# Optimization experiments

Measured on AMD Instinct MI355X. Metric: run time of the kernel, lower is better.

Reference implementation:

```python
import jax, jax.numpy as jnp
import numpy as np
import math

C = 32  # per-head channel dim (init arg c)


def _layernorm(x, g, b, eps=1e-5):
    mu = x.mean(-1, keepdims=True)
    var = ((x - mu) ** 2).mean(-1, keepdims=True)
    return (x - mu) * jax.lax.rsqrt(var + eps) * g + b


def setup_inputs() -> dict:
    key = jax.random.key(0)
    ks = jax.random.split(key, 8)
    S, N, D = 17, 4096, 256  # S = 1 target + 16 MSTA templates
    h = jax.random.normal(ks[0], (S, N, D), jnp.float32)
    msta_mask = jax.random.uniform(ks[1], (S - 1, N)) < 0.5
    # module requires count(target_msta_mask) == count(msta_mask); use equal masks
    target_msta_mask = msta_mask
    w = lambda k: jax.random.normal(k, (D, D), jnp.float32) * 0.05
    return dict(
        h=h, target_msta_mask=target_msta_mask, msta_mask=msta_mask,
        Wq=w(ks[2]), Wk=w(ks[3]), Wv=w(ks[4]), Wo=w(ks[5]),
        bo=jnp.zeros((D,), jnp.float32),
        ln_g=jnp.ones((D,), jnp.float32), ln_b=jnp.zeros((D,), jnp.float32),
    )


def reference(h, target_msta_mask, msta_mask, Wq, Wk, Wv, Wo, bo, ln_g, ln_b):
    S, N, D = h.shape
    H = D // C
    M = msta_mask.shape[0]  # == S - 1
    # --- msta_h[target_msta_mask] = h[1:][msta_mask] (rank-matched scatter, jit-safe) ---
    h1 = h[1:].reshape(M * N, D)
    src = msta_mask.reshape(-1)
    dst = target_msta_mask.reshape(-1)
    src_rank = jnp.cumsum(src.astype(jnp.int32)) - 1
    buf = jnp.zeros((M * N, D), h.dtype).at[jnp.where(src, src_rank, M * N)].set(h1, mode='drop')
    dst_rank = jnp.clip(jnp.cumsum(dst.astype(jnp.int32)) - 1, 0, M * N - 1)
    msta_h = jnp.where(dst[:, None], buf[dst_rank], 0.0).reshape(M, N, D)
    # --- full-column equivalent of the subset attention (per-position independent) ---
    cols = target_msta_mask.any(0)                      # [N]
    attn_h = jnp.concatenate([h[:1], msta_h], axis=0)   # [S, N, D]
    mask = jnp.concatenate([cols[None], target_msta_mask], axis=0)  # [S, N]; == inverse_mask == attn_mask (full cols)
    q = (attn_h @ Wq.T).reshape(S, N, H, C)
    k = (attn_h @ Wk.T).reshape(S, N, H, C)
    v = (attn_h @ Wv.T).reshape(S, N, H, C)
    att = jnp.einsum('snhc,tnhc->stnh', q, k) / math.sqrt(C)
    att = att - (~mask).astype(h.dtype)[None, :, :, None] * 1e9
    att = jax.nn.softmax(att, axis=1)                   # softmax over key-sample axis t
    attn_o = jnp.einsum('stnh,tnhc->snhc', att, v).reshape(S, N, D)
    # o[inverse_mask] = attn_o[attn_mask]  (masks coincide in full-column form)
    o = jnp.where(mask[..., None], attn_o, h @ Wv.T)
    o = o @ Wo.T + bo
    # dropout is identity in eval mode
    return _layernorm(h + o, ln_g, ln_b)
```

## Files before the change

### kernel.cpp

```cpp
#include <hip/hip_runtime.h>
#include <hip/hip_bf16.h>

#define S 17
#define NPOS 4096
#define D 256
#define NH 8
#define CH 32
#define MROWS 16

typedef __attribute__((ext_vector_type(8))) short bf16x8;
typedef __attribute__((ext_vector_type(4))) float f32x4;

__device__ __forceinline__ float bfu(unsigned short u) {
  return __uint_as_float(((unsigned int)u) << 16);
}
__device__ __forceinline__ unsigned short f2b(float f) {
  __hip_bfloat16 t = __float2bfloat16(f);
  return *reinterpret_cast<unsigned short*>(&t);
}
__device__ __forceinline__ void unpack16(const uint4 A, const uint4 B, float* r) {
  r[0]  = __uint_as_float(A.x << 16); r[1]  = __uint_as_float(A.x & 0xffff0000u);
  r[2]  = __uint_as_float(A.y << 16); r[3]  = __uint_as_float(A.y & 0xffff0000u);
  r[4]  = __uint_as_float(A.z << 16); r[5]  = __uint_as_float(A.z & 0xffff0000u);
  r[6]  = __uint_as_float(A.w << 16); r[7]  = __uint_as_float(A.w & 0xffff0000u);
  r[8]  = __uint_as_float(B.x << 16); r[9]  = __uint_as_float(B.x & 0xffff0000u);
  r[10] = __uint_as_float(B.y << 16); r[11] = __uint_as_float(B.y & 0xffff0000u);
  r[12] = __uint_as_float(B.z << 16); r[13] = __uint_as_float(B.z & 0xffff0000u);
  r[14] = __uint_as_float(B.w << 16); r[15] = __uint_as_float(B.w & 0xffff0000u);
}
__device__ __forceinline__ float readv(const void* p, int f32, size_t i) {
  return f32 ? ((const float*)p)[i] : bfu(((const unsigned short*)p)[i]);
}

__device__ __forceinline__ void gl_lds16(const unsigned short* g, unsigned short* l) {
  __builtin_amdgcn_global_load_lds(
      (const __attribute__((address_space(1))) unsigned int*)g,
      (__attribute__((address_space(3))) unsigned int*)l, 16, 0, 0);
}

struct TensorList {
  const unsigned short* p[8];
  int n[8];
};

__global__ void detect_multi_kernel(TensorList tl, int* __restrict__ flags) {
  __shared__ int s_totnz, s_evnz, s_evwild;
  if (threadIdx.x == 0) { s_totnz = 0; s_evnz = 0; s_evwild = 0; }
  __syncthreads();
  const unsigned short* p = tl.p[blockIdx.x];
  const int n = tl.n[blockIdx.x];
  const int w = n < 4096 ? n : 4096;
  int totnz = 0, evnz = 0, evwild = 0;
  for (int i = threadIdx.x; i < w; i += blockDim.x) {
    unsigned short u = p[i];
    if (u) {
      totnz++;
      if (!(i & 1)) {
        evnz++;
        int e = (u >> 7) & 0xFF;
        if (e == 0 || e == 255 || e < 97 || e > 157) evwild++;
      }
    }
  }
  atomicAdd(&s_totnz, totnz);
  atomicAdd(&s_evnz, evnz);
  atomicAdd(&s_evwild, evwild);
  __syncthreads();
  if (threadIdx.x == 0) {
    const int evcount = w / 2;
    int f;
    if (s_totnz == 0) f = 0;
    else if (s_evnz == 0) f = 1;
    else if (s_evwild * 8 > evcount) f = 1;
    else f = 0;
    flags[blockIdx.x] = f;
  }
}

__global__ void detect_mask_kernel(const unsigned int* __restrict__ w,
                                   int* __restrict__ cls) {
  __shared__ int viol[5];
  if (threadIdx.x < 5) viol[threadIdx.x] = 0;
  __syncthreads();
  int v_i32 = 0, v_f32 = 0, v_bf16 = 0, v_u8 = 0, v_i64 = 0;
  const int nwords = 65536 / 4;
  for (int i = threadIdx.x; i < nwords; i += blockDim.x) {
    unsigned int x = w[i];
    if (x > 1u) v_i32 = 1;
    if (x != 0u && x != 0x3F800000u) v_f32 = 1;
    unsigned int lo = x & 0xFFFFu, hi = x >> 16;
    if ((lo != 0u && lo != 0x3F80u) || (hi != 0u && hi != 0x3F80u)) v_bf16 = 1;
    if ((x & 0xFEFEFEFEu) != 0u) v_u8 = 1;
    if ((i & 1) && x != 0u) v_i64 = 1;
  }
  if (v_i32) atomicOr(&viol[0], 1);
  if (v_f32) atomicOr(&viol[1], 1);
  if (v_bf16) atomicOr(&viol[2], 1);
  if (v_u8) atomicOr(&viol[3], 1);
  if (v_i64) atomicOr(&viol[4], 1);
  __syncthreads();
  if (threadIdx.x == 0) {
    int c;
    if (!viol[0] && !viol[4]) c = 4;
    else if (!viol[0]) c = 0;
    else if (!viol[1]) c = 2;
    else if (!viol[2]) c = 3;
    else c = 1;
    *cls = c;
  }
}

__global__ void expand_mask_kernel(const void* __restrict__ tmask, const int* __restrict__ cls,
                                   unsigned char* __restrict__ mask_u8) {
  int n = blockIdx.x * blockDim.x + threadIdx.x;
  if (n >= NPOS) return;
  const int c = *cls;
  int any = 0;
  for (int m = 0; m < MROWS; m++) {
    size_t idx = (size_t)m * NPOS + n;
    int v;
    if (c == 0)      v = ((const int*)tmask)[idx] != 0;
    else if (c == 1) v = ((const unsigned char*)tmask)[idx] != 0;
    else if (c == 2) v = ((const unsigned int*)tmask)[idx] != 0u;
    else if (c == 3) v = ((const unsigned short*)tmask)[idx] != 0u;
    else             v = ((const unsigned long long*)tmask)[idx] != 0ull;
    mask_u8[(m + 1) * NPOS + n] = (unsigned char)v;
    any |= v;
  }
  mask_u8[n] = (unsigned char)any;
}

struct WPtrs { const void* p[4]; };

__global__ void conv_w_kernel(WPtrs wp, const int* __restrict__ flags,
                              unsigned short* __restrict__ w_bf) {
  for (int i = blockIdx.x * blockDim.x + threadIdx.x; i < 4 * 65536;
       i += gridDim.x * blockDim.x) {
    int which = i >> 16, off = i & 65535;
    int f = flags[1 + which];
    w_bf[i] = f ? f2b(((const float*)wp.p[which])[off])
                : ((const unsigned short*)wp.p[which])[off];
  }
}

__global__ __launch_bounds__(256) void qkv_kernel(
    const void* __restrict__ h, const int* __restrict__ flags,
    const unsigned short* __restrict__ w_bf,
    unsigned short* __restrict__ q_ws, unsigned short* __restrict__ k_ws,
    unsigned short* __restrict__ v_ws) {
  __shared__ unsigned short lds[16384];
  const int tid = threadIdx.x;
  const int wave = tid >> 6, lane = tid & 63;
  const int l15 = lane & 15, quad = lane >> 4;
  const int bid = blockIdx.x;
  const int nt = (bid >> 3) % 6;
  const size_t mt = (size_t)(bid & 7) + 8 * (size_t)(bid / 48);
  const size_t R = mt * 128;
  const unsigned short* Wb = w_bf + (size_t)(nt * 128) * 256;
  const int hf32 = flags[0];
  const int srow = lane >> 3;
  const int scol = (lane & 7) * 8;
  const int wm = wave >> 1, wn = wave & 1;

  f32x4 acc[4][4];
  #pragma unroll
  for (int a = 0; a < 4; a++)
    #pragma unroll
    for (int b = 0; b < 4; b++) acc[a][b] = (f32x4){0.f, 0.f, 0.f, 0.f};

  for (int k0 = 0; k0 < 4; k0++) {
    if (hf32) {
      const float* hf = (const float*)h;
      #pragma unroll
      for (int i = 0; i < 4; i++) {
        int row = i * 32 + wave * 8 + srow;
        const float4* src = (const float4*)&hf[(R + row) * 256 + k0 * 64 + scol];
        float4 v0 = src[0], v1 = src[1];
        unsigned int w0 = ((unsigned)f2b(v0.y) << 16) | f2b(v0.x);
        unsigned int w1 = ((unsigned)f2b(v0.w) << 16) | f2b(v0.z);
        unsigned int w2 = ((unsigned)f2b(v1.y) << 16) | f2b(v1.x);
        unsigned int w3 = ((unsigned)f2b(v1.w) << 16) | f2b(v1.z);
        *(uint4*)&lds[i * 2048 + wave * 512 + lane * 8] = make_uint4(w0, w1, w2, w3);
      }
    } else {
      const unsigned short* hb = (const unsigned short*)h;
      #pragma unroll
      for (int i = 0; i < 4; i++) {
        int row = i * 32 + wave * 8 + srow;
        gl_lds16(&hb[(R + row) * 256 + k0 * 64 + scol], &lds[i * 2048 + wave * 512]);
      }
    }
    #pragma unroll
    for (int i = 0; i < 4; i++) {
      int row = i * 32 + wave * 8 + srow;
      gl_lds16(&Wb[(size_t)row * 256 + k0 * 64 + scol], &lds[8192 + i * 2048 + wave * 512]);
    }
    asm volatile("s_waitcnt vmcnt(0)" ::: "memory");
    __syncthreads();
    bf16x8 af[4][2], bfr[4][2];
    #pragma unroll
    for (int mi = 0; mi < 4; mi++)
      #pragma unroll
      for (int kk = 0; kk < 2; kk++)
        af[mi][kk] = *(const bf16x8*)&lds[(wm * 64 + mi * 16 + l15) * 64 + kk * 32 + quad * 8];
    #pragma unroll
    for (int ni = 0; ni < 4; ni++)
      #pragma unroll
      for (int kk = 0; kk < 2; kk++)
        bfr[ni][kk] = *(const bf16x8*)&lds[8192 + (wn * 64 + ni * 16 + l15) * 64 + kk * 32 + quad * 8];
    #pragma unroll
    for (int kk = 0; kk < 2; kk++)
      #pragma unroll
      for (int mi = 0; mi < 4; mi++)
        #pragma unroll
        for (int ni = 0; ni < 4; ni++)
          acc[mi][ni] = __builtin_amdgcn_mfma_f32_16x16x32_bf16(af[mi][kk], bfr[ni][kk],
                                                                acc[mi][ni], 0, 0, 0);
    __syncthreads();
  }
  const int p = nt >> 1;
  const int cbase = (nt & 1) * 128;
  unsigned short* dst = (p == 0) ? q_ws : (p == 1) ? k_ws : v_ws;
  #pragma unroll
  for (int mi = 0; mi < 4; mi++)
    #pragma unroll
    for (int ni = 0; ni < 4; ni++)
      #pragma unroll
      for (int r = 0; r < 4; r++) {
        int row = wm * 64 + mi * 16 + quad * 4 + r;
        int col = cbase + wn * 64 + ni * 16 + l15;
        dst[(R + row) * 256 + col] = f2b(acc[mi][ni][r]);
      }
}

__global__ __launch_bounds__(256) void attn_kernel(
    const unsigned short* __restrict__ q_ws, const unsigned short* __restrict__ k_ws,
    const unsigned short* __restrict__ v_ws, const unsigned char* __restrict__ mask_u8,
    unsigned short* __restrict__ o_ws) {
  __shared__ unsigned short qb[S * D], kb[S * D], vb[S * D];
  __shared__ float pmat[S * 160];
  __shared__ unsigned char sm[32];
  const int tid = threadIdx.x;
  const int n = blockIdx.x;
  if (tid < S) sm[tid] = mask_u8[tid * NPOS + n];
  for (int idx = tid; idx < S * 32; idx += 256) {
    int s = idx >> 5, c = idx & 31;
    size_t g = ((size_t)s * NPOS + n) * 32 + c;
    ((uint4*)qb)[idx] = ((const uint4*)q_ws)[g];
    ((uint4*)kb)[idx] = ((const uint4*)k_ws)[g];
    ((uint4*)vb)[idx] = ((const uint4*)v_ws)[g];
  }
  __syncthreads();
  {
    const int hh = tid >> 5, s = tid & 31;
    if (s < S) {
      float qv[32];
      const uint4* qp = (const uint4*)(qb + s * 256 + hh * 32);
      unpack16(qp[0], qp[1], qv);
      unpack16(qp[2], qp[3], qv + 16);
      const float scale = 0.17677669529663687f;
      float sc[S];
      float mx = -3.4e38f;
      #pragma unroll
      for (int t = 0; t < S; t++) {
        const uint4* kp = (const uint4*)(kb + t * 256 + hh * 32);
        float kv[16];
        unpack16(kp[0], kp[1], kv);
        float a = 0.f;
        #pragma unroll
        for (int u = 0; u < 16; u++) a = fmaf(qv[u], kv[u], a);
        unpack16(kp[2], kp[3], kv);
        #pragma unroll
        for (int u = 0; u < 16; u++) a = fmaf(qv[16 + u], kv[u], a);
        a *= scale;
        if (!sm[t]) a -= 1e9f;
        sc[t] = a;
        mx = fmaxf(mx, a);
      }
      float sum = 0.f;
      #pragma unroll
      for (int t = 0; t < S; t++) { sc[t] = __expf(sc[t] - mx); sum += sc[t]; }
      const float inv = 1.f / sum;
      float* pr = pmat + s * 160 + hh * 20;
      #pragma unroll
      for (int t = 0; t < S; t++) pr[t] = sc[t] * inv;
      pr[17] = 0.f; pr[18] = 0.f; pr[19] = 0.f;
    }
  }
  __syncthreads();
  {
    const int d = tid, hh = d >> 5;
    float vf[S];
    #pragma unroll
    for (int t = 0; t < S; t++) vf[t] = bfu(vb[t * 256 + d]);
    #pragma unroll 1
    for (int s = 0; s < S; s++) {
      const float* pr = pmat + s * 160 + hh * 20;
      float ov = 0.f;
      #pragma unroll
      for (int t = 0; t < S; t++) ov = fmaf(pr[t], vf[t], ov);
      const float o_val = sm[s] ? ov : vf[s];
      o_ws[((size_t)s * NPOS + n) * 256 + d] = f2b(o_val);
    }
  }
}

template <int HF32>
__device__ __forceinline__ void oproj_body(
    const unsigned short* __restrict__ o_ws, const void* __restrict__ h,
    const unsigned short* __restrict__ w_bf, const int* __restrict__ fl,
    const void* __restrict__ bo, const void* __restrict__ lng,
    const void* __restrict__ lnb, float* __restrict__ out,
    unsigned short* lds) {
  const int tid = threadIdx.x;
  const int wave = tid >> 6, lane = tid & 63;
  const int l15 = lane & 15, quad = lane >> 4;
  const int srow = lane >> 3;
  const int scol = (lane & 7) * 8;
  const size_t R = (size_t)blockIdx.x * 128;
  const unsigned short* Wp = w_bf + 3 * 65536;

  f32x4 acc0[16], acc1[16];
  #pragma unroll
  for (int j = 0; j < 16; j++) {
    acc0[j] = (f32x4){0.f, 0.f, 0.f, 0.f};
    acc1[j] = (f32x4){0.f, 0.f, 0.f, 0.f};
  }

  for (int k0 = 0; k0 < 4; k0++) {
    #pragma unroll
    for (int i = 0; i < 4; i++) {
      int row = i * 32 + wave * 8 + srow;
      gl_lds16(&o_ws[(R + row) * 256 + k0 * 64 + scol], &lds[i * 2048 + wave * 512]);
    }
    #pragma unroll
    for (int i = 0; i < 8; i++) {
      int row = i * 32 + wave * 8 + srow;
      gl_lds16(&Wp[(size_t)row * 256 + k0 * 64 + scol], &lds[8192 + i * 2048 + wave * 512]);
    }
    asm volatile("s_waitcnt vmcnt(0)" ::: "memory");
    __syncthreads();
    bf16x8 af0k[2], af1k[2];
    #pragma unroll
    for (int kk = 0; kk < 2; kk++) {
      af0k[kk] = *(const bf16x8*)&lds[(wave * 32 + l15) * 64 + kk * 32 + quad * 8];
      af1k[kk] = *(const bf16x8*)&lds[(wave * 32 + 16 + l15) * 64 + kk * 32 + quad * 8];
    }
    #pragma unroll
    for (int kk = 0; kk < 2; kk++)
      #pragma unroll
      for (int j = 0; j < 16; j++) {
        bf16x8 b = *(const bf16x8*)&lds[8192 + (j * 16 + l15) * 64 + kk * 32 + quad * 8];
        acc0[j] = __builtin_amdgcn_mfma_f32_16x16x32_bf16(af0k[kk], b, acc0[j], 0, 0, 0);
        acc1[j] = __builtin_amdgcn_mfma_f32_16x16x32_bf16(af1k[kk], b, acc1[j], 0, 0, 0);
      }
    __syncthreads();
  }

  const int f5 = fl[5], f6 = fl[6], f7 = fl[7];
  float xsum0[4] = {0, 0, 0, 0}, xsq0[4] = {0, 0, 0, 0};
  float xsum1[4] = {0, 0, 0, 0}, xsq1[4] = {0, 0, 0, 0};
  #pragma unroll
  for (int j = 0; j < 16; j++) {
    const int col = j * 16 + l15;
    const float boj = readv(bo, f5, col);
    #pragma unroll
    for (int r = 0; r < 4; r++) {
      const size_t row0 = R + wave * 32 + quad * 4 + r;
      const size_t row1 = row0 + 16;
      float h0 = HF32 ? ((const float*)h)[row0 * 256 + col]
                      : bfu(((const unsigned short*)h)[row0 * 256 + col]);
      float h1 = HF32 ? ((const float*)h)[row1 * 256 + col]
                      : bfu(((const unsigned short*)h)[row1 * 256 + col]);
      float x0 = acc0[j][r] + h0 + boj;
      float x1 = acc1[j][r] + h1 + boj;
      acc0[j][r] = x0; acc1[j][r] = x1;
      xsum0[r] += x0; xsq0[r] += x0 * x0;
      xsum1[r] += x1; xsq1[r] += x1 * x1;
    }
  }
  #pragma unroll
  for (int r = 0; r < 4; r++) {
    #pragma unroll
    for (int m = 1; m <= 8; m <<= 1) {
      xsum0[r] += __shfl_xor(xsum0[r], m, 64);
      xsq0[r]  += __shfl_xor(xsq0[r], m, 64);
      xsum1[r] += __shfl_xor(xsum1[r], m, 64);
      xsq1[r]  += __shfl_xor(xsq1[r], m, 64);
    }
  }
  float mu0[4], rs0[4], mu1[4], rs1[4];
  #pragma unroll
  for (int r = 0; r < 4; r++) {
    mu0[r] = xsum0[r] * (1.0f / 256.0f);
    rs0[r] = rsqrtf(fmaxf(xsq0[r] * (1.0f / 256.0f) - mu0[r] * mu0[r], 0.0f) + 1e-5f);
    mu1[r] = xsum1[r] * (1.0f / 256.0f);
    rs1[r] = rsqrtf(fmaxf(xsq1[r] * (1.0f / 256.0f) - mu1[r] * mu1[r], 0.0f) + 1e-5f);
  }
  #pragma unroll
  for (int j = 0; j < 16; j++) {
    const int col = j * 16 + l15;
    const float gj = readv(lng, f6, col);
    const float bj = readv(lnb, f7, col);
    #pragma unroll
    for (int r = 0; r < 4; r++) {
      const size_t row0 = R + wave * 32 + quad * 4 + r;
      out[row0 * 256 + col] = (acc0[j][r] - mu0[r]) * rs0[r] * gj + bj;
      out[(row0 + 16) * 256 + col] = (acc1[j][r] - mu1[r]) * rs1[r] * gj + bj;
    }
  }
}

__global__ __launch_bounds__(256) void oproj_ln_kernel(
    const unsigned short* __restrict__ o_ws, const void* __restrict__ h,
    const unsigned short* __restrict__ w_bf, const int* __restrict__ flags,
    const void* __restrict__ bo, const void* __restrict__ lng,
    const void* __restrict__ lnb, float* __restrict__ out) {
  __shared__ unsigned short lds[24576];
  if (flags[0]) oproj_body<1>(o_ws, h, w_bf, flags, bo, lng, lnb, out, lds);
  else          oproj_body<0>(o_ws, h, w_bf, flags, bo, lng, lnb, out, lds);
}

extern "C" void kernel_launch(void* const* d_in, const int* in_sizes, int n_in,
                              void* d_out, int out_size, void* d_ws, size_t ws_size,
                              hipStream_t stream) {
  const void* h     = d_in[0];
  const void* tmask = d_in[1];
  const void* Wq  = d_in[3];
  const void* Wk  = d_in[4];
  const void* Wv  = d_in[5];
  const void* Wo  = d_in[6];
  const void* bo  = d_in[7];
  const void* lng = d_in[8];
  const void* lnb = d_in[9];
  float* out = (float*)d_out;

  char* ws = (char*)d_ws;
  int* mcls  = (int*)ws;
  int* flags = (int*)(ws + 64);
  unsigned char* mask_u8 = (unsigned char*)(ws + 4096);
  unsigned short* w_bf = (unsigned short*)(ws + 73728);
  unsigned short* q_ws = (unsigned short*)(ws + 598016);
  unsigned short* k_ws = (unsigned short*)(ws + 598016 + 35651584ull);
  unsigned short* v_ws = (unsigned short*)(ws + 598016 + 2 * 35651584ull);
  unsigned short* o_ws = q_ws;

  TensorList tl;
  tl.p[0] = (const unsigned short*)h;   tl.n[0] = in_sizes[0];
  tl.p[1] = (const unsigned short*)Wq;  tl.n[1] = in_sizes[3];
  tl.p[2] = (const unsigned short*)Wk;  tl.n[2] = in_sizes[4];
  tl.p[3] = (const unsigned short*)Wv;  tl.n[3] = in_sizes[5];
  tl.p[4] = (const unsigned short*)Wo;  tl.n[4] = in_sizes[6];
  tl.p[5] = (const unsigned short*)bo;  tl.n[5] = in_sizes[7];
  tl.p[6] = (const unsigned short*)lng; tl.n[6] = in_sizes[8];
  tl.p[7] = (const unsigned short*)lnb; tl.n[7] = in_sizes[9];
  WPtrs wp;
  wp.p[0] = Wq; wp.p[1] = Wk; wp.p[2] = Wv; wp.p[3] = Wo;

  detect_multi_kernel<<<8, 256, 0, stream>>>(tl, flags);
  detect_mask_kernel<<<1, 256, 0, stream>>>((const unsigned int*)tmask, mcls);
  expand_mask_kernel<<<NPOS / 256, 256, 0, stream>>>(tmask, mcls, mask_u8);
  conv_w_kernel<<<256, 256, 0, stream>>>(wp, flags, w_bf);
  qkv_kernel<<<544 * 6, 256, 0, stream>>>(h, flags, w_bf, q_ws, k_ws, v_ws);
  attn_kernel<<<NPOS, 256, 0, stream>>>(q_ws, k_ws, v_ws, mask_u8, o_ws);
  oproj_ln_kernel<<<S * NPOS / 128, 256, 0, stream>>>(o_ws, h, w_bf, flags,
                                                      bo, lng, lnb, out);
}
```

Measured before the change: 384.0 us.

## Enlarge QKV GEMM tile to 256 rows and merge preprocessing launches

The QKV projection block grows from 256 to 512 threads and from 128 to 256 rows per block, sharing each loaded 128-column weight tile across twice as many rows. This halves weight traffic per output and halves the block count. The four small setup kernels (dtype detection, mask detection, mask expansion, weight conversion) are merged into two launches to cut launch overhead. The explicit vmcnt wait before the barrier after the LDS-direct global loads was also dropped, which risks a race unless the compiler inserts that wait itself.

```diff
diff --git a/kernel.cpp b/kernel.cpp
--- a/kernel.cpp
+++ b/kernel.cpp
@@ -43,119 +43,120 @@
   int n[8];
 };
 
-__global__ void detect_multi_kernel(TensorList tl, int* __restrict__ flags) {
-  __shared__ int s_totnz, s_evnz, s_evwild;
-  if (threadIdx.x == 0) { s_totnz = 0; s_evnz = 0; s_evwild = 0; }
-  __syncthreads();
-  const unsigned short* p = tl.p[blockIdx.x];
-  const int n = tl.n[blockIdx.x];
-  const int w = n < 4096 ? n : 4096;
-  int totnz = 0, evnz = 0, evwild = 0;
-  for (int i = threadIdx.x; i < w; i += blockDim.x) {
-    unsigned short u = p[i];
-    if (u) {
-      totnz++;
-      if (!(i & 1)) {
-        evnz++;
-        int e = (u >> 7) & 0xFF;
-        if (e == 0 || e == 255 || e < 97 || e > 157) evwild++;
-      }
-    }
-  }
-  atomicAdd(&s_totnz, totnz);
-  atomicAdd(&s_evnz, evnz);
-  atomicAdd(&s_evwild, evwild);
-  __syncthreads();
-  if (threadIdx.x == 0) {
-    const int evcount = w / 2;
-    int f;
-    if (s_totnz == 0) f = 0;
-    else if (s_evnz == 0) f = 1;
-    else if (s_evwild * 8 > evcount) f = 1;
-    else f = 0;
-    flags[blockIdx.x] = f;
-  }
-}
-
-__global__ void detect_mask_kernel(const unsigned int* __restrict__ w,
-                                   int* __restrict__ cls) {
-  __shared__ int viol[5];
-  if (threadIdx.x < 5) viol[threadIdx.x] = 0;
-  __syncthreads();
-  int v_i32 = 0, v_f32 = 0, v_bf16 = 0, v_u8 = 0, v_i64 = 0;
-  const int nwords = 65536 / 4;
-  for (int i = threadIdx.x; i < nwords; i += blockDim.x) {
-    unsigned int x = w[i];
-    if (x > 1u) v_i32 = 1;
-    if (x != 0u && x != 0x3F800000u) v_f32 = 1;
-    unsigned int lo = x & 0xFFFFu, hi = x >> 16;
-    if ((lo != 0u && lo != 0x3F80u) || (hi != 0u && hi != 0x3F80u)) v_bf16 = 1;
-    if ((x & 0xFEFEFEFEu) != 0u) v_u8 = 1;
-    if ((i & 1) && x != 0u) v_i64 = 1;
-  }
-  if (v_i32) atomicOr(&viol[0], 1);
-  if (v_f32) atomicOr(&viol[1], 1);
-  if (v_bf16) atomicOr(&viol[2], 1);
-  if (v_u8) atomicOr(&viol[3], 1);
-  if (v_i64) atomicOr(&viol[4], 1);
-  __syncthreads();
-  if (threadIdx.x == 0) {
-    int c;
-    if (!viol[0] && !viol[4]) c = 4;
-    else if (!viol[0]) c = 0;
-    else if (!viol[1]) c = 2;
-    else if (!viol[2]) c = 3;
-    else c = 1;
-    *cls = c;
-  }
-}
-
-__global__ void expand_mask_kernel(const void* __restrict__ tmask, const int* __restrict__ cls,
-                                   unsigned char* __restrict__ mask_u8) {
-  int n = blockIdx.x * blockDim.x + threadIdx.x;
-  if (n >= NPOS) return;
-  const int c = *cls;
-  int any = 0;
-  for (int m = 0; m < MROWS; m++) {
-    size_t idx = (size_t)m * NPOS + n;
-    int v;
-    if (c == 0)      v = ((const int*)tmask)[idx] != 0;
-    else if (c == 1) v = ((const unsigned char*)tmask)[idx] != 0;
-    else if (c == 2) v = ((const unsigned int*)tmask)[idx] != 0u;
-    else if (c == 3) v = ((const unsigned short*)tmask)[idx] != 0u;
-    else             v = ((const unsigned long long*)tmask)[idx] != 0ull;
-    mask_u8[(m + 1) * NPOS + n] = (unsigned char)v;
-    any |= v;
-  }
-  mask_u8[n] = (unsigned char)any;
+__global__ void detect_kernel(TensorList tl, int* __restrict__ flags,
+                              const unsigned int* __restrict__ mw, int* __restrict__ cls) {
+  if (blockIdx.x < 8) {
+    __shared__ int s_totnz, s_evnz, s_evwild;
+    if (threadIdx.x == 0) { s_totnz = 0; s_evnz = 0; s_evwild = 0; }
+    __syncthreads();
+    const unsigned short* p = tl.p[blockIdx.x];
+    const int n = tl.n[blockIdx.x];
+    const int w = n < 4096 ? n : 4096;
+    int totnz = 0, evnz = 0, evwild = 0;
+    for (int i = threadIdx.x; i < w; i += blockDim.x) {
+      unsigned short u = p[i];
+      if (u) {
+        totnz++;
+        if (!(i & 1)) {
+          evnz++;
+          int e = (u >> 7) & 0xFF;
+          if (e == 0 || e == 255 || e < 97 || e > 157) evwild++;
+        }
+      }
+    }
+    atomicAdd(&s_totnz, totnz);
+    atomicAdd(&s_evnz, evnz);
+    atomicAdd(&s_evwild, evwild);
+    __syncthreads();
+    if (threadIdx.x == 0) {
+      const int evcount = w / 2;
+      int f;
+      if (s_totnz == 0) f = 0;
+      else if (s_evnz == 0) f = 1;
+      else if (s_evwild * 8 > evcount) f = 1;
+      else f = 0;
+      flags[blockIdx.x] = f;
+    }
+  } else {
+    __shared__ int viol[5];
+    if (threadIdx.x < 5) viol[threadIdx.x] = 0;
+    __syncthreads();
+    int v_i32 = 0, v_f32 = 0, v_bf16 = 0, v_u8 = 0, v_i64 = 0;
+    const int nwords = 65536 / 4;
+    for (int i = threadIdx.x; i < nwords; i += blockDim.x) {
+      unsigned int x = mw[i];
+      if (x > 1u) v_i32 = 1;
+      if (x != 0u && x != 0x3F800000u) v_f32 = 1;
+      unsigned int lo = x & 0xFFFFu, hi = x >> 16;
+      if ((lo != 0u && lo != 0x3F80u) || (hi != 0u && hi != 0x3F80u)) v_bf16 = 1;
+      if ((x & 0xFEFEFEFEu) != 0u) v_u8 = 1;
+      if ((i & 1) && x != 0u) v_i64 = 1;
+    }
+    if (v_i32) atomicOr(&viol[0], 1);
+    if (v_f32) atomicOr(&viol[1], 1);
+    if (v_bf16) atomicOr(&viol[2], 1);
+    if (v_u8) atomicOr(&viol[3], 1);
+    if (v_i64) atomicOr(&viol[4], 1);
+    __syncthreads();
+    if (threadIdx.x == 0) {
+      int c;
+      if (!viol[0] && !viol[4]) c = 4;
+      else if (!viol[0]) c = 0;
+      else if (!viol[1]) c = 2;
+      else if (!viol[2]) c = 3;
+      else c = 1;
+      *cls = c;
+    }
+  }
 }
 
 struct WPtrs { const void* p[4]; };
 
-__global__ void conv_w_kernel(WPtrs wp, const int* __restrict__ flags,
-                              unsigned short* __restrict__ w_bf) {
-  for (int i = blockIdx.x * blockDim.x + threadIdx.x; i < 4 * 65536;
-       i += gridDim.x * blockDim.x) {
-    int which = i >> 16, off = i & 65535;
-    int f = flags[1 + which];
-    w_bf[i] = f ? f2b(((const float*)wp.p[which])[off])
-                : ((const unsigned short*)wp.p[which])[off];
-  }
-}
-
-__global__ __launch_bounds__(256) void qkv_kernel(
+__global__ void prep_kernel(const void* __restrict__ tmask, const int* __restrict__ cls,
+                            unsigned char* __restrict__ mask_u8,
+                            WPtrs wp, const int* __restrict__ flags,
+                            unsigned short* __restrict__ w_bf) {
+  if (blockIdx.x < 16) {
+    int n = blockIdx.x * blockDim.x + threadIdx.x;
+    if (n >= NPOS) return;
+    const int c = *cls;
+    int any = 0;
+    for (int m = 0; m < MROWS; m++) {
+      size_t idx = (size_t)m * NPOS + n;
+      int v;
+      if (c == 0)      v = ((const int*)tmask)[idx] != 0;
+      else if (c == 1) v = ((const unsigned char*)tmask)[idx] != 0;
+      else if (c == 2) v = ((const unsigned int*)tmask)[idx] != 0u;
+      else if (c == 3) v = ((const unsigned short*)tmask)[idx] != 0u;
+      else             v = ((const unsigned long long*)tmask)[idx] != 0ull;
+      mask_u8[(m + 1) * NPOS + n] = (unsigned char)v;
+      any |= v;
+    }
+    mask_u8[n] = (unsigned char)any;
+  } else {
+    for (int i = (blockIdx.x - 16) * blockDim.x + threadIdx.x; i < 4 * 65536;
+         i += 256 * 256) {
+      int which = i >> 16, off = i & 65535;
+      int f = flags[1 + which];
+      w_bf[i] = f ? f2b(((const float*)wp.p[which])[off])
+                  : ((const unsigned short*)wp.p[which])[off];
+    }
+  }
+}
+
+__global__ __launch_bounds__(512, 5) void qkv_kernel(
     const void* __restrict__ h, const int* __restrict__ flags,
     const unsigned short* __restrict__ w_bf,
     unsigned short* __restrict__ q_ws, unsigned short* __restrict__ k_ws,
     unsigned short* __restrict__ v_ws) {
-  __shared__ unsigned short lds[16384];
+  __shared__ unsigned short lds[24576];
   const int tid = threadIdx.x;
   const int wave = tid >> 6, lane = tid & 63;
   const int l15 = lane & 15, quad = lane >> 4;
   const int bid = blockIdx.x;
   const int nt = (bid >> 3) % 6;
   const size_t mt = (size_t)(bid & 7) + 8 * (size_t)(bid / 48);
-  const size_t R = mt * 128;
+  const size_t R = mt * 256;
   const unsigned short* Wb = w_bf + (size_t)(nt * 128) * 256;
   const int hf32 = flags[0];
   const int srow = lane >> 3;
@@ -173,29 +174,28 @@
       const float* hf = (const float*)h;
       #pragma unroll
       for (int i = 0; i < 4; i++) {
-        int row = i * 32 + wave * 8 + srow;
+        int row = i * 64 + wave * 8 + srow;
         const float4* src = (const float4*)&hf[(R + row) * 256 + k0 * 64 + scol];
         float4 v0 = src[0], v1 = src[1];
         unsigned int w0 = ((unsigned)f2b(v0.y) << 16) | f2b(v0.x);
         unsigned int w1 = ((unsigned)f2b(v0.w) << 16) | f2b(v0.z);
         unsigned int w2 = ((unsigned)f2b(v1.y) << 16) | f2b(v1.x);
         unsigned int w3 = ((unsigned)f2b(v1.w) << 16) | f2b(v1.z);
-        *(uint4*)&lds[i * 2048 + wave * 512 + lane * 8] = make_uint4(w0, w1, w2, w3);
+        *(uint4*)&lds[i * 4096 + wave * 512 + lane * 8] = make_uint4(w0, w1, w2, w3);
       }
     } else {
       const unsigned short* hb = (const unsigned short*)h;
       #pragma unroll
       for (int i = 0; i < 4; i++) {
-        int row = i * 32 + wave * 8 + srow;
-        gl_lds16(&hb[(R + row) * 256 + k0 * 64 + scol], &lds[i * 2048 + wave * 512]);
-      }
-    }
-    #pragma unroll
-    for (int i = 0; i < 4; i++) {
-      int row = i * 32 + wave * 8 + srow;
-      gl_lds16(&Wb[(size_t)row * 256 + k0 * 64 + scol], &lds[8192 + i * 2048 + wave * 512]);
-    }
-    asm volatile("s_waitcnt vmcnt(0)" ::: "memory");
+        int row = i * 64 + wave * 8 + srow;
+        gl_lds16(&hb[(R + row) * 256 + k0 * 64 + scol], &lds[i * 4096 + wave * 512]);
+      }
+    }
+    #pragma unroll
+    for (int i = 0; i < 2; i++) {
+      int row = i * 64 + wave * 8 + srow;
+      gl_lds16(&Wb[(size_t)row * 256 + k0 * 64 + scol], &lds[16384 + i * 4096 + wave * 512]);
+    }
     __syncthreads();
     bf16x8 af[4][2], bfr[4][2];
     #pragma unroll
@@ -207,7 +207,7 @@
     for (int ni = 0; ni < 4; ni++)
       #pragma unroll
       for (int kk = 0; kk < 2; kk++)
-        bfr[ni][kk] = *(const bf16x8*)&lds[8192 + (wn * 64 + ni * 16 + l15) * 64 + kk * 32 + quad * 8];
+        bfr[ni][kk] = *(const bf16x8*)&lds[16384 + (wn * 64 + ni * 16 + l15) * 64 + kk * 32 + quad * 8];
     #pragma unroll
     for (int kk = 0; kk < 2; kk++)
       #pragma unroll
@@ -457,11 +457,9 @@
   WPtrs wp;
   wp.p[0] = Wq; wp.p[1] = Wk; wp.p[2] = Wv; wp.p[3] = Wo;
 
-  detect_multi_kernel<<<8, 256, 0, stream>>>(tl, flags);
-  detect_mask_kernel<<<1, 256, 0, stream>>>((const unsigned int*)tmask, mcls);
-  expand_mask_kernel<<<NPOS / 256, 256, 0, stream>>>(tmask, mcls, mask_u8);
-  conv_w_kernel<<<256, 256, 0, stream>>>(wp, flags, w_bf);
-  qkv_kernel<<<544 * 6, 256, 0, stream>>>(h, flags, w_bf, q_ws, k_ws, v_ws);
+  detect_kernel<<<9, 256, 0, stream>>>(tl, flags, (const unsigned int*)tmask, mcls);
+  prep_kernel<<<272, 256, 0, stream>>>(tmask, mcls, mask_u8, wp, flags, w_bf);
+  qkv_kernel<<<272 * 6, 512, 0, stream>>>(h, flags, w_bf, q_ws, k_ws, v_ws);
   attn_kernel<<<NPOS, 256, 0, stream>>>(q_ws, k_ws, v_ws, mask_u8, o_ws);
   oproj_ln_kernel<<<S * NPOS / 128, 256, 0, stream>>>(o_ws, h, w_bf, flags,
                                                       bo, lng, lnb, out);
```

Result: slower. 467.4 us (+21.7%).
